# Performance work log

Measured on AMD Instinct MI355X. Metric: run time of the kernel, lower is better.

Reference implementation:

```python
import jax, jax.numpy as jnp
import numpy as np

N = 100000   # graph nodes (TSP edges)
E = 600000   # graph edges
IN_DIM = 2; HID = 128; HEADS = 16; DH = HID // HEADS
L = 4; FF = 2 * HID; OUT = 1
EPS = 1e-5; SLOPE = 0.2  # BatchNorm eps, GAT leaky_relu slope


def _mlp(x, W1, b1, W2, b2):
    return jnp.maximum(x @ W1 + b1, 0.0) @ W2 + b2


def _bn(x, g, b):
    # BatchNorm1d in training mode: batch (node-dim) statistics, biased variance
    mu = x.mean(0)
    var = x.var(0)
    return (x - mu) * jax.lax.rsqrt(var + EPS) * g + b


def _gat(h, src, dst, W, al, ar, bias):
    # DGL GATConv: per-head projection, additive attention, edge softmax over incoming edges
    z = (h @ W).reshape(N, HEADS, DH)          # [N,H,Dh]
    el = (z * al).sum(-1)                      # [N,H] source term
    er = (z * ar).sum(-1)                      # [N,H] dest term
    e = jax.nn.leaky_relu(el[src] + er[dst], SLOPE)            # [E,H]
    m = jax.ops.segment_max(e, dst, num_segments=N)            # [N,H]
    a = jnp.exp(e - m[dst])                                    # [E,H]
    denom = jax.ops.segment_sum(a, dst, num_segments=N)        # [N,H]
    msg = jax.ops.segment_sum(a[:, :, None] * z[src], dst, num_segments=N)  # [N,H,Dh]
    out = msg / jnp.where(denom > 0, denom, 1.0)[:, :, None]
    return out.reshape(N, HID) + bias


def _forward(x, src, dst,
             emb_W1, emb_b1, emb_W2, emb_b2, emb_Ws, emb_bs,
             gat_W, gat_al, gat_ar, gat_b, bn1_g, bn1_b,
             ff_W1, ff_b1, ff_W2, ff_b2, bn2_g, bn2_b,
             dec_W1, dec_b1, dec_W2, dec_b2):
    # embed MLP with skip connection
    h = _mlp(x, emb_W1, emb_b1, emb_W2, emb_b2) + (x @ emb_Ws + emb_bs)
    xs = [h]
    for l in range(L):  # fixed small layer count
        a = _gat(h, src, dst, gat_W[l], gat_al[l], gat_ar[l], gat_b[l])
        h = _bn(h + a, bn1_g[l], bn1_b[l])
        f = _mlp(h, ff_W1[l], ff_b1[l], ff_W2[l], ff_b2[l])
        h = _bn(h + f, bn2_g[l], bn2_b[l])
        xs.append(h)
    hc = jnp.concatenate(xs, axis=-1)  # JumpingKnowledge 'cat' -> [N, HID*(L+1)]
    return _mlp(hc, dec_W1, dec_b1, dec_W2, dec_b2)


def setup_inputs() -> dict:
    key = jax.random.key(0)
    ks = jax.random.split(key, 20)
    w = lambda k, shape: jax.random.normal(k, shape, jnp.float32) * 0.05
    x = jax.random.normal(ks[0], (N, IN_DIM), jnp.float32)
    src = jax.random.randint(ks[1], (E,), 0, N)
    # guarantee every node has at least one incoming edge
    dst = jnp.concatenate([jnp.arange(N), jax.random.randint(ks[2], (E - N,), 0, N)])
    return {
        'x': x, 'src': src, 'dst': dst,
        'emb_W1': w(ks[3], (IN_DIM, HID)), 'emb_b1': jnp.zeros((HID,), jnp.float32),
        'emb_W2': w(ks[4], (HID, HID)),    'emb_b2': jnp.zeros((HID,), jnp.float32),
        'emb_Ws': w(ks[5], (IN_DIM, HID)), 'emb_bs': jnp.zeros((HID,), jnp.float32),
        'gat_W': w(ks[6], (L, HID, HID)),
        'gat_al': w(ks[7], (L, HEADS, DH)), 'gat_ar': w(ks[8], (L, HEADS, DH)),
        'gat_b': jnp.zeros((L, HID), jnp.float32),
        'bn1_g': jnp.ones((L, HID), jnp.float32), 'bn1_b': jnp.zeros((L, HID), jnp.float32),
        'ff_W1': w(ks[9], (L, HID, FF)),  'ff_b1': jnp.zeros((L, FF), jnp.float32),
        'ff_W2': w(ks[10], (L, FF, HID)), 'ff_b2': jnp.zeros((L, HID), jnp.float32),
        'bn2_g': jnp.ones((L, HID), jnp.float32), 'bn2_b': jnp.zeros((L, HID), jnp.float32),
        'dec_W1': w(ks[11], (HID * (L + 1), HID)), 'dec_b1': jnp.zeros((HID,), jnp.float32),
        'dec_W2': w(ks[12], (HID, OUT)),           'dec_b2': jnp.zeros((OUT,), jnp.float32),
    }


def reference(x, src, dst,
              emb_W1, emb_b1, emb_W2, emb_b2, emb_Ws, emb_bs,
              gat_W, gat_al, gat_ar, gat_b, bn1_g, bn1_b,
              ff_W1, ff_b1, ff_W2, ff_b2, bn2_g, bn2_b,
              dec_W1, dec_b1, dec_W2, dec_b2):
    return _forward(x, src, dst,
                    emb_W1, emb_b1, emb_W2, emb_b2, emb_Ws, emb_bs,
                    gat_W, gat_al, gat_ar, gat_b, bn1_g, bn1_b,
                    ff_W1, ff_b1, ff_W2, ff_b2, bn2_g, bn2_b,
                    dec_W1, dec_b1, dec_W2, dec_b2)
```

## Files before the change

### kernel.cpp

```cpp
#include <hip/hip_runtime.h>
#include <math.h>

typedef __attribute__((ext_vector_type(8))) short bf16x8;
typedef __attribute__((ext_vector_type(4))) float f32x4;

struct BN5 {
    const float* st[5];
    const float* g[5];
    const float* b[5];
    const float* stR;
    const float* gR;
    const float* bR;
    float invN;
};

static __device__ __forceinline__ short f2bf(float f) {
    unsigned u = __float_as_uint(f);
    unsigned r = (u + 0x7fffu + ((u >> 16) & 1u)) >> 16;
    return (short)r;
}
static __device__ __forceinline__ float bf2f(short s) {
    return __uint_as_float(((unsigned)(unsigned short)s) << 16);
}
static __device__ __forceinline__ float bflo(int v) { return bf2f((short)(v & 0xffff)); }
static __device__ __forceinline__ float bfhi(int v) { return bf2f((short)(((unsigned)v) >> 16)); }
static __device__ __forceinline__ int pack2(float a, float b) {
    return (int)(((unsigned)(unsigned short)f2bf(b) << 16) | (unsigned)(unsigned short)f2bf(a));
}

__global__ void zero_i32_k(int* __restrict__ p, int n) {
    int i = blockIdx.x * 256 + threadIdx.x;
    if (i < n) p[i] = 0;
}

__global__ __launch_bounds__(256) void wconv_k(const float* __restrict__ W, short* __restrict__ Wt,
                                               int K, int Nc) {
    int slice = blockIdx.y;
    const float* src = W + (size_t)slice * K * Nc;
    short* dst = Wt + (size_t)slice * K * Nc;
    int idx = blockIdx.x * 256 + threadIdx.x;
    if (idx >= K * Nc) return;
    int k = idx / Nc, n = idx - k * Nc;
    dst[(size_t)n * K + k] = f2bf(src[idx]);
}

__global__ __launch_bounds__(256) void embed_k(
    const float* __restrict__ x, const float* __restrict__ W1, const float* __restrict__ b1,
    const float* __restrict__ Ws, const float* __restrict__ bs,
    int* __restrict__ u2, int* __restrict__ h2, int Nn)
{
    int idx = blockIdx.x * 256 + threadIdx.x;
    if (idx >= Nn * 64) return;
    int n = idx >> 6, c = (idx & 63) * 2;
    float x0 = x[2*n], x1 = x[2*n+1];
    float u0 = fmaxf(fmaf(x1, W1[128+c],   fmaf(x0, W1[c],   b1[c])),   0.f);
    float u1 = fmaxf(fmaf(x1, W1[128+c+1], fmaf(x0, W1[c+1], b1[c+1])), 0.f);
    float h0 = fmaf(x1, Ws[128+c],   fmaf(x0, Ws[c],   bs[c]));
    float h1 = fmaf(x1, Ws[128+c+1], fmaf(x0, Ws[c+1], bs[c+1]));
    u2[idx] = pack2(u0, u1);
    h2[idx] = pack2(h0, h1);
}

template<int NK, int RELU, int BETA, int ELR>
__global__ __launch_bounds__(256) void gemm2_k(
    const short* __restrict__ A0, const short* __restrict__ A1,
    const short* __restrict__ A2, const short* __restrict__ A3,
    const short* __restrict__ A4, int Astr,
    const short* __restrict__ Wt, int ldWt,
    const float* __restrict__ bias, short* __restrict__ C, const short* __restrict__ Rres,
    int Nrows, int ldC, BN5 bn,
    const float* __restrict__ al, const float* __restrict__ ar,
    float* __restrict__ elo, float* __restrict__ ero)
{
    __shared__ short Bs[128][136];
    const int row0 = blockIdx.x * 128;
    const int col0 = blockIdx.y * 128;
    const int t = threadIdx.x;
    const int w = t >> 6, lane = t & 63, q = lane >> 4, m = lane & 15;

    f32x4 acc[2][8];
    #pragma unroll
    for (int rb = 0; rb < 2; ++rb)
        #pragma unroll
        for (int cb = 0; cb < 8; ++cb)
            acc[rb][cb] = (f32x4){0.f, 0.f, 0.f, 0.f};

    const short* Asrc[5] = {A0, A1, A2, A3, A4};
    int rr0 = row0 + w*32 + m;      if (rr0 > Nrows - 1) rr0 = Nrows - 1;
    int rr1 = row0 + w*32 + 16 + m; if (rr1 > Nrows - 1) rr1 = Nrows - 1;

    #pragma unroll
    for (int kh = 0; kh < NK; ++kh) {
        if (kh) __syncthreads();
        #pragma unroll
        for (int it = 0; it < 8; ++it) {
            int ci = t + it * 256;
            int r = ci >> 4, j = (ci & 15) * 8;
            *(int4*)&Bs[r][j] = *(const int4*)(Wt + (size_t)(col0 + r) * ldWt + kh * 128 + j);
        }
        const short* pa0 = Asrc[kh] + (size_t)rr0 * Astr + q * 8;
        const short* pa1 = Asrc[kh] + (size_t)rr1 * Astr + q * 8;
        bf16x8 af0[4], af1[4];
        #pragma unroll
        for (int ks = 0; ks < 4; ++ks) {
            af0[ks] = *(const bf16x8*)(pa0 + ks * 32);
            af1[ks] = *(const bf16x8*)(pa1 + ks * 32);
        }
        if (bn.st[kh]) {
            const float* st = bn.st[kh];
            const float* gg = bn.g[kh];
            const float* bb = bn.b[kh];
            #pragma unroll
            for (int ks = 0; ks < 4; ++ks) {
                #pragma unroll
                for (int e = 0; e < 8; ++e) {
                    int c = ks * 32 + q * 8 + e;
                    float mu = st[c] * bn.invN;
                    float var = st[128 + c] * bn.invN - mu * mu;
                    float sc = rsqrtf(var + 1e-5f) * gg[c];
                    float bc = bb[c] - mu * sc;
                    af0[ks][e] = f2bf(fmaf(bf2f(af0[ks][e]), sc, bc));
                    af1[ks][e] = f2bf(fmaf(bf2f(af1[ks][e]), sc, bc));
                }
            }
        }
        __syncthreads();
        #pragma unroll
        for (int ks = 0; ks < 4; ++ks) {
            bf16x8 bfr[8];
            #pragma unroll
            for (int cb = 0; cb < 8; ++cb)
                bfr[cb] = *(const bf16x8*)&Bs[cb * 16 + m][ks * 32 + q * 8];
            #pragma unroll
            for (int cb = 0; cb < 8; ++cb) {
                acc[0][cb] = __builtin_amdgcn_mfma_f32_16x16x32_bf16(af0[ks], bfr[cb], acc[0][cb], 0, 0, 0);
                acc[1][cb] = __builtin_amdgcn_mfma_f32_16x16x32_bf16(af1[ks], bfr[cb], acc[1][cb], 0, 0, 0);
            }
        }
    }

    __syncthreads();
    short* Cs = (short*)Bs;
    #pragma unroll
    for (int rb = 0; rb < 2; ++rb) {
        #pragma unroll
        for (int r = 0; r < 4; ++r) {
            int lrow = w * 32 + rb * 16 + q * 4 + r;
            #pragma unroll
            for (int cb = 0; cb < 8; ++cb) {
                float v = acc[rb][cb][r];
                if (bias) v += bias[col0 + cb * 16 + m];
                if (RELU) v = fmaxf(v, 0.f);
                Cs[lrow * 132 + cb * 16 + m] = f2bf(v);
            }
        }
    }
    __syncthreads();
    const int chunk = t & 15, rgrp = t >> 4, cb8 = chunk * 8;
    const short* Rd = Rres ? Rres : C;
    #pragma unroll
    for (int j = 0; j < 8; ++j) {
        int r = rgrp + j * 16;
        int grow = row0 + r;
        if (grow < Nrows) {
            int2 u0 = *(const int2*)(Cs + r * 132 + cb8);
            int2 u1 = *(const int2*)(Cs + r * 132 + cb8 + 4);
            int4 cv = make_int4(u0.x, u0.y, u1.x, u1.y);
            size_t gb = (size_t)grow * ldC + col0 + cb8;
            if (BETA) {
                int4 rv = *(const int4*)(Rd + gb);
                int* cp = (int*)&cv; const int* rp = (const int*)&rv;
                #pragma unroll
                for (int e = 0; e < 4; ++e)
                    cp[e] = pack2(bflo(cp[e]) + bflo(rp[e]), bfhi(cp[e]) + bfhi(rp[e]));
            }
            *(int4*)(C + gb) = cv;
            if (ELR) {
                const int* cp = (const int*)&cv;
                float sl = 0.f, sr = 0.f;
                #pragma unroll
                for (int e = 0; e < 4; ++e) {
                    float lo = bflo(cp[e]), hi = bfhi(cp[e]);
                    sl = fmaf(lo, al[cb8 + 2*e], sl); sl = fmaf(hi, al[cb8 + 2*e + 1], sl);
                    sr = fmaf(lo, ar[cb8 + 2*e], sr); sr = fmaf(hi, ar[cb8 + 2*e + 1], sr);
                }
                elo[(size_t)grow * 16 + chunk] = sl;
                ero[(size_t)grow * 16 + chunk] = sr;
            }
        }
    }
}

__global__ __launch_bounds__(256) void ff_fused_k(
    const short* __restrict__ T1,
    const short* __restrict__ W1t,
    const short* __restrict__ W2t,
    const float* __restrict__ b1, const float* __restrict__ b2,
    const float* __restrict__ st1, const float* __restrict__ g1, const float* __restrict__ bb1,
    float invN, short* __restrict__ C, int Nrows, float* __restrict__ statsOut)
{
    __shared__ short Wbuf[128][136];
    __shared__ short Fbuf[128 * 132];
    const int row0 = blockIdx.x * 128;
    const int t = threadIdx.x;
    const int w = t >> 6, lane = t & 63, q = lane >> 4, m = lane & 15;

    f32x4 acc2[2][8];
    #pragma unroll
    for (int rb = 0; rb < 2; ++rb)
        #pragma unroll
        for (int cb = 0; cb < 8; ++cb)
            acc2[rb][cb] = (f32x4){0.f, 0.f, 0.f, 0.f};

    int rr0 = row0 + w*32 + m;      if (rr0 > Nrows - 1) rr0 = Nrows - 1;
    int rr1 = row0 + w*32 + 16 + m; if (rr1 > Nrows - 1) rr1 = Nrows - 1;

    bf16x8 af0[4], af1[4];
    {
        const short* pa0 = T1 + (size_t)rr0 * 128 + q * 8;
        const short* pa1 = T1 + (size_t)rr1 * 128 + q * 8;
        #pragma unroll
        for (int ks = 0; ks < 4; ++ks) {
            af0[ks] = *(const bf16x8*)(pa0 + ks * 32);
            af1[ks] = *(const bf16x8*)(pa1 + ks * 32);
        }
        #pragma unroll
        for (int ks = 0; ks < 4; ++ks) {
            #pragma unroll
            for (int e = 0; e < 8; ++e) {
                int c = ks * 32 + q * 8 + e;
                float mu = st1[c] * invN;
                float var = st1[128 + c] * invN - mu * mu;
                float sc = rsqrtf(var + 1e-5f) * g1[c];
                float bc = bb1[c] - mu * sc;
                af0[ks][e] = f2bf(fmaf(bf2f(af0[ks][e]), sc, bc));
                af1[ks][e] = f2bf(fmaf(bf2f(af1[ks][e]), sc, bc));
            }
        }
    }

    #pragma unroll
    for (int half = 0; half < 2; ++half) {
        if (half) __syncthreads();
        #pragma unroll
        for (int it = 0; it < 8; ++it) {
            int ci = t + it * 256;
            int r = ci >> 4, j = (ci & 15) * 8;
            *(int4*)&Wbuf[r][j] = *(const int4*)(W1t + (size_t)(half * 128 + r) * 128 + j);
        }
        __syncthreads();
        f32x4 acc1[2][8];
        #pragma unroll
        for (int rb = 0; rb < 2; ++rb)
            #pragma unroll
            for (int cb = 0; cb < 8; ++cb)
                acc1[rb][cb] = (f32x4){0.f, 0.f, 0.f, 0.f};
        #pragma unroll
        for (int ks = 0; ks < 4; ++ks) {
            bf16x8 bfr[8];
            #pragma unroll
            for (int cb = 0; cb < 8; ++cb)
                bfr[cb] = *(const bf16x8*)&Wbuf[cb * 16 + m][ks * 32 + q * 8];
            #pragma unroll
            for (int cb = 0; cb < 8; ++cb) {
                acc1[0][cb] = __builtin_amdgcn_mfma_f32_16x16x32_bf16(af0[ks], bfr[cb], acc1[0][cb], 0, 0, 0);
                acc1[1][cb] = __builtin_amdgcn_mfma_f32_16x16x32_bf16(af1[ks], bfr[cb], acc1[1][cb], 0, 0, 0);
            }
        }
        #pragma unroll
        for (int rb = 0; rb < 2; ++rb) {
            #pragma unroll
            for (int r = 0; r < 4; ++r) {
                int lrow = w * 32 + rb * 16 + q * 4 + r;
                #pragma unroll
                for (int cb = 0; cb < 8; ++cb) {
                    float v = acc1[rb][cb][r] + b1[half * 128 + cb * 16 + m];
                    Fbuf[lrow * 132 + cb * 16 + m] = f2bf(fmaxf(v, 0.f));
                }
            }
        }
        __syncthreads();
        #pragma unroll
        for (int it = 0; it < 8; ++it) {
            int ci = t + it * 256;
            int r = ci >> 4, j = (ci & 15) * 8;
            *(int4*)&Wbuf[r][j] = *(const int4*)(W2t + (size_t)r * 256 + half * 128 + j);
        }
        __syncthreads();
        const short* fa0 = Fbuf + (w * 32 + m) * 132 + q * 8;
        const short* fa1 = Fbuf + (w * 32 + 16 + m) * 132 + q * 8;
        #pragma unroll
        for (int ks = 0; ks < 4; ++ks) {
            bf16x8 ga0 = *(const bf16x8*)(fa0 + ks * 32);
            bf16x8 ga1 = *(const bf16x8*)(fa1 + ks * 32);
            bf16x8 bfr[8];
            #pragma unroll
            for (int cb = 0; cb < 8; ++cb)
                bfr[cb] = *(const bf16x8*)&Wbuf[cb * 16 + m][ks * 32 + q * 8];
            #pragma unroll
            for (int cb = 0; cb < 8; ++cb) {
                acc2[0][cb] = __builtin_amdgcn_mfma_f32_16x16x32_bf16(ga0, bfr[cb], acc2[0][cb], 0, 0, 0);
                acc2[1][cb] = __builtin_amdgcn_mfma_f32_16x16x32_bf16(ga1, bfr[cb], acc2[1][cb], 0, 0, 0);
            }
        }
    }

    __syncthreads();
    #pragma unroll
    for (int rb = 0; rb < 2; ++rb) {
        #pragma unroll
        for (int r = 0; r < 4; ++r) {
            int lrow = w * 32 + rb * 16 + q * 4 + r;
            #pragma unroll
            for (int cb = 0; cb < 8; ++cb) {
                float v = acc2[rb][cb][r] + b2[cb * 16 + m];
                Fbuf[lrow * 132 + cb * 16 + m] = f2bf(v);
            }
        }
    }
    __syncthreads();
    const int chunk = t & 15, rgrp = t >> 4, cb8 = chunk * 8;
    float scR[8], bbR[8];
    #pragma unroll
    for (int e = 0; e < 8; ++e) {
        int c = cb8 + e;
        float mu = st1[c] * invN;
        float var = st1[128 + c] * invN - mu * mu;
        float sc = rsqrtf(var + 1e-5f) * g1[c];
        scR[e] = sc; bbR[e] = bb1[c] - mu * sc;
    }
    float sS[8], sQ[8];
    #pragma unroll
    for (int e = 0; e < 8; ++e) { sS[e] = 0.f; sQ[e] = 0.f; }
    #pragma unroll
    for (int j = 0; j < 8; ++j) {
        int r = rgrp + j * 16;
        int grow = row0 + r;
        if (grow < Nrows) {
            int2 u0 = *(const int2*)(Fbuf + r * 132 + cb8);
            int2 u1 = *(const int2*)(Fbuf + r * 132 + cb8 + 4);
            int4 cv = make_int4(u0.x, u0.y, u1.x, u1.y);
            size_t gb = (size_t)grow * 128 + cb8;
            int4 rv = *(const int4*)(T1 + gb);
            int* cp = (int*)&cv; const int* rp = (const int*)&rv;
            #pragma unroll
            for (int e = 0; e < 4; ++e) {
                float rlo = fmaf(bflo(rp[e]), scR[2*e],   bbR[2*e]);
                float rhi = fmaf(bfhi(rp[e]), scR[2*e+1], bbR[2*e+1]);
                float lo = bflo(cp[e]) + rlo;
                float hi = bfhi(cp[e]) + rhi;
                cp[e] = pack2(lo, hi);
                lo = bflo(cp[e]); hi = bfhi(cp[e]);
                sS[2*e]   += lo; sQ[2*e]   += lo * lo;
                sS[2*e+1] += hi; sQ[2*e+1] += hi * hi;
            }
            *(int4*)(C + gb) = cv;
        }
    }
    __syncthreads();
    float* fs = (float*)Wbuf;
    #pragma unroll
    for (int e = 0; e < 8; ++e) {
        fs[rgrp * 128 + cb8 + e]        = sS[e];
        fs[2048 + rgrp * 128 + cb8 + e] = sQ[e];
    }
    __syncthreads();
    if (t < 128) {
        float a = 0.f;
        #pragma unroll
        for (int g = 0; g < 16; ++g) a += fs[g * 128 + t];
        atomicAdd(&statsOut[t], a);
    } else {
        int c = t - 128;
        float a = 0.f;
        #pragma unroll
        for (int g = 0; g < 16; ++g) a += fs[2048 + g * 128 + c];
        atomicAdd(&statsOut[128 + c], a);
    }
}

__global__ void count_k(const int* __restrict__ dst, int* __restrict__ cnt, int E) {
    int e = blockIdx.x * 256 + threadIdx.x;
    if (e < E) atomicAdd(&cnt[dst[e]], 1);
}

__global__ __launch_bounds__(256) void scan_part_k(const int* __restrict__ cnt,
                                                   int* __restrict__ bsum, int Nn) {
    __shared__ int red[256];
    int base = blockIdx.x * 1024;
    int s = 0;
    for (int i = threadIdx.x; i < 1024; i += 256) {
        int g = base + i;
        if (g < Nn) s += cnt[g];
    }
    red[threadIdx.x] = s; __syncthreads();
    for (int off = 128; off; off >>= 1) {
        if ((int)threadIdx.x < off) red[threadIdx.x] += red[threadIdx.x + off];
        __syncthreads();
    }
    if (threadIdx.x == 0) bsum[blockIdx.x] = red[0];
}

__global__ __launch_bounds__(256) void scan_top_k(int* __restrict__ bsum, int nb) {
    __shared__ int buf[256];
    int v = ((int)threadIdx.x < nb) ? bsum[threadIdx.x] : 0;
    buf[threadIdx.x] = v; __syncthreads();
    for (int off = 1; off < 256; off <<= 1) {
        int tv = ((int)threadIdx.x >= off) ? buf[threadIdx.x - off] : 0;
        __syncthreads();
        buf[threadIdx.x] += tv;
        __syncthreads();
    }
    if ((int)threadIdx.x < nb) bsum[threadIdx.x] = buf[threadIdx.x] - v;
}

__global__ __launch_bounds__(256) void scan_fin_k(const int* __restrict__ cnt,
    const int* __restrict__ bsum, int* __restrict__ rowptr, int* __restrict__ wpos, int Nn)
{
    __shared__ int tsum[256];
    int base = blockIdx.x * 1024;
    int g0 = base + (int)threadIdx.x * 4;
    int v[4]; int s = 0;
    #pragma unroll
    for (int j = 0; j < 4; ++j) {
        int g = g0 + j;
        v[j] = (g < Nn) ? cnt[g] : 0;
        s += v[j];
    }
    tsum[threadIdx.x] = s; __syncthreads();
    for (int off = 1; off < 256; off <<= 1) {
        int tv = ((int)threadIdx.x >= off) ? tsum[threadIdx.x - off] : 0;
        __syncthreads();
        tsum[threadIdx.x] += tv;
        __syncthreads();
    }
    int run = bsum[blockIdx.x] + tsum[threadIdx.x] - s;
    #pragma unroll
    for (int j = 0; j < 4; ++j) {
        int g = g0 + j;
        if (g < Nn) { wpos[g] = run; rowptr[g + 1] = run + v[j]; }
        run += v[j];
    }
    if (blockIdx.x == 0 && threadIdx.x == 0) rowptr[0] = 0;
}

__global__ void scatter_k(const int* __restrict__ src, const int* __restrict__ dst,
                          int* __restrict__ wpos, int* __restrict__ esrc, int E) {
    int e = blockIdx.x * 256 + threadIdx.x;
    if (e < E) {
        int p = atomicAdd(&wpos[dst[e]], 1);
        esrc[p] = src[e];
    }
}

__global__ __launch_bounds__(256) void gat_k(
    const short* __restrict__ h, const short* __restrict__ z,
    const float* __restrict__ el, const float* __restrict__ er,
    const int* __restrict__ rowptr, const int* __restrict__ esrc,
    const float* __restrict__ gbias, short* __restrict__ t1, int Nn,
    const float* __restrict__ hstats, const float* __restrict__ hg,
    const float* __restrict__ hb, float invN)
{
    int gw = (blockIdx.x * 256 + threadIdx.x) >> 6;
    if (gw >= Nn) return;
    int lane = threadIdx.x & 63;
    int c = lane * 2;
    int head = lane >> 2;
    float ern = er[gw*16 + head];
    int beg = rowptr[gw], end = rowptr[gw+1];
    float m = -3.0e38f, den = 0.f, a0 = 0.f, a1 = 0.f;
    int i = beg;
    for (; i + 3 < end; i += 4) {
        int s0 = esrc[i], s1 = esrc[i+1], s2 = esrc[i+2], s3 = esrc[i+3];
        float e0 = el[s0*16 + head] + ern;
        float e1 = el[s1*16 + head] + ern;
        float e2 = el[s2*16 + head] + ern;
        float e3 = el[s3*16 + head] + ern;
        int zz0 = *(const int*)(z + (size_t)s0*128 + c);
        int zz1 = *(const int*)(z + (size_t)s1*128 + c);
        int zz2 = *(const int*)(z + (size_t)s2*128 + c);
        int zz3 = *(const int*)(z + (size_t)s3*128 + c);
        e0 = (e0 > 0.f) ? e0 : 0.2f * e0;
        e1 = (e1 > 0.f) ? e1 : 0.2f * e1;
        e2 = (e2 > 0.f) ? e2 : 0.2f * e2;
        e3 = (e3 > 0.f) ? e3 : 0.2f * e3;
        float nm = fmaxf(fmaxf(fmaxf(e0, e1), fmaxf(e2, e3)), m);
        float sc = __expf(m - nm);
        float w0 = __expf(e0 - nm), w1 = __expf(e1 - nm);
        float w2 = __expf(e2 - nm), w3 = __expf(e3 - nm);
        den = fmaf(den, sc, (w0 + w1) + (w2 + w3));
        a0 = fmaf(a0, sc, fmaf(w0, bflo(zz0), fmaf(w1, bflo(zz1), fmaf(w2, bflo(zz2), w3 * bflo(zz3)))));
        a1 = fmaf(a1, sc, fmaf(w0, bfhi(zz0), fmaf(w1, bfhi(zz1), fmaf(w2, bfhi(zz2), w3 * bfhi(zz3)))));
        m = nm;
    }
    for (; i + 1 < end; i += 2) {
        int s0 = esrc[i], s1 = esrc[i+1];
        float e0 = el[s0*16 + head] + ern;
        float e1 = el[s1*16 + head] + ern;
        int zz0 = *(const int*)(z + (size_t)s0*128 + c);
        int zz1 = *(const int*)(z + (size_t)s1*128 + c);
        e0 = (e0 > 0.f) ? e0 : 0.2f * e0;
        e1 = (e1 > 0.f) ? e1 : 0.2f * e1;
        float nm = fmaxf(m, fmaxf(e0, e1));
        float sc = __expf(m - nm);
        float w0 = __expf(e0 - nm);
        float w1 = __expf(e1 - nm);
        den = fmaf(den, sc, w0 + w1);
        a0  = fmaf(a0, sc, fmaf(w0, bflo(zz0), w1 * bflo(zz1)));
        a1  = fmaf(a1, sc, fmaf(w0, bfhi(zz0), w1 * bfhi(zz1)));
        m = nm;
    }
    if (i < end) {
        int s0 = esrc[i];
        float e0 = el[s0*16 + head] + ern;
        int zz0 = *(const int*)(z + (size_t)s0*128 + c);
        e0 = (e0 > 0.f) ? e0 : 0.2f * e0;
        float nm = fmaxf(m, e0);
        float sc = __expf(m - nm);
        float w0 = __expf(e0 - nm);
        den = fmaf(den, sc, w0);
        a0  = fmaf(a0, sc, w0 * bflo(zz0));
        a1  = fmaf(a1, sc, w0 * bfhi(zz0));
    }
    float inv = 1.f / den;
    size_t o = (size_t)gw*64 + lane;
    int hv = ((const int*)h)[o];
    float h0 = bflo(hv), h1 = bfhi(hv);
    if (hstats) {
        float mu0 = hstats[c] * invN;
        float v0  = hstats[128+c] * invN - mu0*mu0;
        float s0  = rsqrtf(v0 + 1e-5f) * hg[c];
        h0 = fmaf(h0 - mu0, s0, hb[c]);
        float mu1 = hstats[c+1] * invN;
        float v1  = hstats[128+c+1] * invN - mu1*mu1;
        float s1  = rsqrtf(v1 + 1e-5f) * hg[c+1];
        h1 = fmaf(h1 - mu1, s1, hb[c+1]);
    }
    float r0 = h0 + a0*inv + gbias[c];
    float r1 = h1 + a1*inv + gbias[c+1];
    ((int*)t1)[o] = pack2(r0, r1);
}

__global__ __launch_bounds__(256) void bn_stats_k(const short* __restrict__ xin,
    float* __restrict__ stats, int Nn)
{
    __shared__ float s0s[256], s1s[256], q0s[256], q1s[256];
    int pair = threadIdx.x & 63;
    int slot = threadIdx.x >> 6;
    float s0 = 0.f, s1 = 0.f, q0 = 0.f, q1 = 0.f;
    for (int r = blockIdx.x*4 + slot; r < Nn; r += gridDim.x*4) {
        int v = *(const int*)(xin + (size_t)r*128 + pair*2);
        float a = bflo(v), b = bfhi(v);
        s0 += a; s1 += b;
        q0 = fmaf(a, a, q0); q1 = fmaf(b, b, q1);
    }
    s0s[threadIdx.x] = s0; s1s[threadIdx.x] = s1;
    q0s[threadIdx.x] = q0; q1s[threadIdx.x] = q1;
    __syncthreads();
    if (slot == 0) {
        #pragma unroll
        for (int j = 1; j < 4; ++j) {
            s0 += s0s[pair + j*64]; s1 += s1s[pair + j*64];
            q0 += q0s[pair + j*64]; q1 += q1s[pair + j*64];
        }
        atomicAdd(&stats[pair*2],       s0);
        atomicAdd(&stats[pair*2+1],     s1);
        atomicAdd(&stats[128+pair*2],   q0);
        atomicAdd(&stats[128+pair*2+1], q1);
    }
}

__global__ __launch_bounds__(256) void dec_out_k(const short* __restrict__ udec,
    const float* __restrict__ W2, const float* __restrict__ b2,
    float* __restrict__ out, int Nn)
{
    int gw = (blockIdx.x * 256 + threadIdx.x) >> 6;
    if (gw >= Nn) return;
    int lane = threadIdx.x & 63;
    int v = ((const int*)(udec + (size_t)gw * 128))[lane];
    float p = bflo(v) * W2[lane*2] + bfhi(v) * W2[lane*2 + 1];
    #pragma unroll
    for (int off = 32; off > 0; off >>= 1) p += __shfl_down(p, off);
    if (lane == 0) out[gw] = p + b2[0];
}

extern "C" void kernel_launch(void* const* d_in, const int* in_sizes, int n_in,
                              void* d_out, int out_size, void* d_ws, size_t ws_size,
                              hipStream_t stream)
{
    const float* x      = (const float*)d_in[0];
    const int*   src    = (const int*)  d_in[1];
    const int*   dst    = (const int*)  d_in[2];
    const float* emb_W1 = (const float*)d_in[3];
    const float* emb_b1 = (const float*)d_in[4];
    const float* emb_W2 = (const float*)d_in[5];
    const float* emb_b2 = (const float*)d_in[6];
    const float* emb_Ws = (const float*)d_in[7];
    const float* emb_bs = (const float*)d_in[8];
    const float* gat_W  = (const float*)d_in[9];
    const float* gat_al = (const float*)d_in[10];
    const float* gat_ar = (const float*)d_in[11];
    const float* gat_b  = (const float*)d_in[12];
    const float* bn1_g  = (const float*)d_in[13];
    const float* bn1_b  = (const float*)d_in[14];
    const float* ff_W1  = (const float*)d_in[15];
    const float* ff_b1  = (const float*)d_in[16];
    const float* ff_W2  = (const float*)d_in[17];
    const float* ff_b2  = (const float*)d_in[18];
    const float* bn2_g  = (const float*)d_in[19];
    const float* bn2_b  = (const float*)d_in[20];
    const float* dec_W1 = (const float*)d_in[21];
    const float* dec_b1 = (const float*)d_in[22];
    const float* dec_W2 = (const float*)d_in[23];
    const float* dec_b2 = (const float*)d_in[24];
    float* out = (float*)d_out;
    (void)n_in; (void)out_size;

    const int N = in_sizes[0] / 2;
    const int E = in_sizes[1];
    const float invN = 1.f / (float)N;

    char* p = (char*)d_ws;
    size_t used = 0;
    auto carve = [&](size_t bytes) {
        char* r = p; size_t a = (bytes + 255) & ~(size_t)255;
        p += a; used += a; return r;
    };
    const size_t nbH = (size_t)N * 128 * 2;
    short* xs[5];
    for (int i = 0; i < 5; ++i) xs[i] = (short*)carve(nbH);
    short* t1   = (short*)carve(nbH);
    char*  big  = (char*)carve(2 * nbH);
    int*   cnt    = (int*)carve((size_t)N * 4);
    float* stats8 = (float*)carve(8 * 256 * 4);
    int*   rowptr = (int*)carve((size_t)(N + 1) * 4);
    int*   wpos   = (int*)carve((size_t)N * 4);
    int*   esrc   = (int*)carve((size_t)E * 4);
    int*   bsum   = (int*)carve(256 * 4);
    short* emb_W2t = (short*)carve((size_t)128 * 128 * 2);
    short* gat_Wt  = (short*)carve((size_t)4 * 128 * 128 * 2);
    short* ff_W1t  = (short*)carve((size_t)4 * 128 * 256 * 2);
    short* ff_W2t  = (short*)carve((size_t)4 * 256 * 128 * 2);
    short* dec_W1t = (short*)carve((size_t)640 * 128 * 2);
    if (used > ws_size) return;

    short* u    = (short*)big;
    short* z    = (short*)big;
    float* el   = (float*)(big + nbH);
    float* er   = el + (size_t)N * 16;
    short* udec = (short*)big;

    dim3 b256(256);
    int ecb  = (E + 255) / 256;
    int nel2 = (N * 64 + 255) / 256;
    int gx   = (N + 127) / 128;
    int nwv  = (N + 3) / 4;
    int nb   = (N + 1023) / 1024;

    BN5 bn0;
    for (int i = 0; i < 5; ++i) { bn0.st[i] = nullptr; bn0.g[i] = nullptr; bn0.b[i] = nullptr; }
    bn0.stR = nullptr; bn0.gR = nullptr; bn0.bR = nullptr; bn0.invN = invN;

    wconv_k<<<dim3(64, 1), b256, 0, stream>>>(emb_W2, emb_W2t, 128, 128);
    wconv_k<<<dim3(64, 4), b256, 0, stream>>>(gat_W,  gat_Wt,  128, 128);
    wconv_k<<<dim3(128, 4), b256, 0, stream>>>(ff_W1, ff_W1t,  128, 256);
    wconv_k<<<dim3(128, 4), b256, 0, stream>>>(ff_W2, ff_W2t,  256, 128);
    wconv_k<<<dim3(320, 1), b256, 0, stream>>>(dec_W1, dec_W1t, 640, 128);

    {
        int ztot = (int)(((char*)(stats8 + 8*256) - (char*)cnt) / 4);
        zero_i32_k<<<(ztot + 255) / 256, b256, 0, stream>>>(cnt, ztot);
    }

    count_k<<<ecb, b256, 0, stream>>>(dst, cnt, E);
    scan_part_k<<<nb, b256, 0, stream>>>(cnt, bsum, N);
    scan_top_k<<<1, b256, 0, stream>>>(bsum, nb);
    scan_fin_k<<<nb, b256, 0, stream>>>(cnt, bsum, rowptr, wpos, N);
    scatter_k<<<ecb, b256, 0, stream>>>(src, dst, wpos, esrc, E);

    embed_k<<<nel2, b256, 0, stream>>>(x, emb_W1, emb_b1, emb_Ws, emb_bs, (int*)u, (int*)xs[0], N);
    gemm2_k<1,0,1,0><<<dim3(gx,1), b256, 0, stream>>>(u,u,u,u,u, 128, emb_W2t, 128,
        emb_b2, xs[0], nullptr, N, 128, bn0, nullptr, nullptr, nullptr, nullptr);

    for (int l = 0; l < 4; ++l) {
        float* st1 = stats8 + (size_t)(l*2)   * 256;
        float* st2 = stats8 + (size_t)(l*2+1) * 256;
        short* hl = xs[l];
        const float* hst = (l == 0) ? nullptr : stats8 + (size_t)((l-1)*2+1) * 256;
        const float* hgp = (l == 0) ? nullptr : bn2_g + (l-1)*128;
        const float* hbp = (l == 0) ? nullptr : bn2_b + (l-1)*128;

        BN5 bz = bn0; bz.st[0] = hst; bz.g[0] = hgp; bz.b[0] = hbp;
        gemm2_k<1,0,0,1><<<dim3(gx,1), b256, 0, stream>>>(hl,hl,hl,hl,hl, 128,
            gat_Wt + (size_t)l*128*128, 128, nullptr, z, nullptr, N, 128, bz,
            gat_al + l*128, gat_ar + l*128, el, er);
        gat_k<<<nwv, b256, 0, stream>>>(hl, z, el, er, rowptr, esrc, gat_b + l*128, t1, N,
                                        hst, hgp, hbp, invN);
        bn_stats_k<<<400, b256, 0, stream>>>(t1, st1, N);
        ff_fused_k<<<gx, b256, 0, stream>>>(t1,
            ff_W1t + (size_t)l*128*256, ff_W2t + (size_t)l*256*128,
            ff_b1 + l*256, ff_b2 + l*128,
            st1, bn1_g + l*128, bn1_b + l*128, invN,
            xs[l+1], N, st2);
    }

    BN5 bd = bn0;
    for (int k = 1; k < 5; ++k) {
        bd.st[k] = stats8 + (size_t)((k-1)*2+1) * 256;
        bd.g[k]  = bn2_g + (k-1)*128;
        bd.b[k]  = bn2_b + (k-1)*128;
    }
    gemm2_k<5,1,0,0><<<dim3(gx,1), b256, 0, stream>>>(xs[0], xs[1], xs[2], xs[3], xs[4], 128,
        dec_W1t, 640, dec_b1, udec, nullptr, N, 128, bd,
        nullptr, nullptr, nullptr, nullptr);
    dec_out_k<<<nwv, b256, 0, stream>>>(udec, dec_W2, dec_b2, out, N);
}
```

Before: 1.062 ms.

## Fuse decoder output projection into decoder GEMM and shrink FF kernel LDS

The decoder's final 128->1 projection now runs in the epilogue of the decoder GEMM as a per-row dot product with a shared-memory reduction. This removes the write and re-read of the intermediate decoder activations and one kernel launch. The fused FF kernel now processes its hidden dimension in four 64-wide quarters instead of two 128-wide halves, which reduces its shared memory and register footprint. It also declares launch bounds of three blocks per CU to raise occupancy, at the cost of more barriers and W-tile reloads.

```diff
diff --git a/kernel.cpp b/kernel.cpp
--- a/kernel.cpp
+++ b/kernel.cpp
@@ -8,9 +8,6 @@
     const float* st[5];
     const float* g[5];
     const float* b[5];
-    const float* stR;
-    const float* gR;
-    const float* bR;
     float invN;
 };
 
@@ -61,7 +58,7 @@
     h2[idx] = pack2(h0, h1);
 }
 
-template<int NK, int RELU, int BETA, int ELR>
+template<int NK, int RELU, int BETA, int ELR, int DEC>
 __global__ __launch_bounds__(256) void gemm2_k(
     const short* __restrict__ A0, const short* __restrict__ A1,
     const short* __restrict__ A2, const short* __restrict__ A3,
@@ -70,7 +67,8 @@
     const float* __restrict__ bias, short* __restrict__ C, const short* __restrict__ Rres,
     int Nrows, int ldC, BN5 bn,
     const float* __restrict__ al, const float* __restrict__ ar,
-    float* __restrict__ elo, float* __restrict__ ero)
+    float* __restrict__ elo, float* __restrict__ ero,
+    const float* __restrict__ dW2, const float* __restrict__ db2, float* __restrict__ dout)
 {
     __shared__ short Bs[128][136];
     const int row0 = blockIdx.x * 128;
@@ -158,6 +156,11 @@
     __syncthreads();
     const int chunk = t & 15, rgrp = t >> 4, cb8 = chunk * 8;
     const short* Rd = Rres ? Rres : C;
+    float dp[8];
+    if (DEC) {
+        #pragma unroll
+        for (int j = 0; j < 8; ++j) dp[j] = 0.f;
+    }
     #pragma unroll
     for (int j = 0; j < 8; ++j) {
         int r = rgrp + j * 16;
@@ -174,7 +177,7 @@
                 for (int e = 0; e < 4; ++e)
                     cp[e] = pack2(bflo(cp[e]) + bflo(rp[e]), bfhi(cp[e]) + bfhi(rp[e]));
             }
-            *(int4*)(C + gb) = cv;
+            if (!DEC) *(int4*)(C + gb) = cv;
             if (ELR) {
                 const int* cp = (const int*)&cv;
                 float sl = 0.f, sr = 0.f;
@@ -187,11 +190,38 @@
                 elo[(size_t)grow * 16 + chunk] = sl;
                 ero[(size_t)grow * 16 + chunk] = sr;
             }
-        }
-    }
-}
-
-__global__ __launch_bounds__(256) void ff_fused_k(
+            if (DEC) {
+                const int* cp = (const int*)&cv;
+                float s = 0.f;
+                #pragma unroll
+                for (int e = 0; e < 4; ++e) {
+                    s = fmaf(bflo(cp[e]), dW2[cb8 + 2*e],     s);
+                    s = fmaf(bfhi(cp[e]), dW2[cb8 + 2*e + 1], s);
+                }
+                dp[j] = s;
+            }
+        }
+    }
+    if (DEC) {
+        __syncthreads();
+        float* red = (float*)Bs;
+        #pragma unroll
+        for (int j = 0; j < 8; ++j)
+            red[(rgrp + j * 16) * 16 + chunk] = dp[j];
+        __syncthreads();
+        if (t < 128) {
+            int grow = row0 + t;
+            if (grow < Nrows) {
+                float s = 0.f;
+                #pragma unroll
+                for (int g = 0; g < 16; ++g) s += red[t * 16 + g];
+                dout[grow] = s + db2[0];
+            }
+        }
+    }
+}
+
+__global__ __launch_bounds__(256, 3) void ff_fused_k(
     const short* __restrict__ T1,
     const short* __restrict__ W1t,
     const short* __restrict__ W2t,
@@ -199,8 +229,9 @@
     const float* __restrict__ st1, const float* __restrict__ g1, const float* __restrict__ bb1,
     float invN, short* __restrict__ C, int Nrows, float* __restrict__ statsOut)
 {
-    __shared__ short Wbuf[128][136];
-    __shared__ short Fbuf[128 * 132];
+    __shared__ short smem[17920];
+    short* Wb = smem;
+    short* Fb = smem + 9216;
     const int row0 = blockIdx.x * 128;
     const int t = threadIdx.x;
     const int w = t >> 6, lane = t & 63, q = lane >> 4, m = lane & 15;
@@ -239,30 +270,29 @@
         }
     }
 
-    #pragma unroll
-    for (int half = 0; half < 2; ++half) {
-        if (half) __syncthreads();
-        #pragma unroll
-        for (int it = 0; it < 8; ++it) {
+    for (int qt = 0; qt < 4; ++qt) {
+        if (qt) __syncthreads();
+        #pragma unroll
+        for (int it = 0; it < 4; ++it) {
             int ci = t + it * 256;
             int r = ci >> 4, j = (ci & 15) * 8;
-            *(int4*)&Wbuf[r][j] = *(const int4*)(W1t + (size_t)(half * 128 + r) * 128 + j);
-        }
-        __syncthreads();
-        f32x4 acc1[2][8];
+            *(int4*)&Wb[r * 136 + j] = *(const int4*)(W1t + (size_t)(qt * 64 + r) * 128 + j);
+        }
+        __syncthreads();
+        f32x4 acc1[2][4];
         #pragma unroll
         for (int rb = 0; rb < 2; ++rb)
             #pragma unroll
-            for (int cb = 0; cb < 8; ++cb)
+            for (int cb = 0; cb < 4; ++cb)
                 acc1[rb][cb] = (f32x4){0.f, 0.f, 0.f, 0.f};
         #pragma unroll
         for (int ks = 0; ks < 4; ++ks) {
-            bf16x8 bfr[8];
-            #pragma unroll
-            for (int cb = 0; cb < 8; ++cb)
-                bfr[cb] = *(const bf16x8*)&Wbuf[cb * 16 + m][ks * 32 + q * 8];
-            #pragma unroll
-            for (int cb = 0; cb < 8; ++cb) {
+            bf16x8 bfr[4];
+            #pragma unroll
+            for (int cb = 0; cb < 4; ++cb)
+                bfr[cb] = *(const bf16x8*)&Wb[(cb * 16 + m) * 136 + ks * 32 + q * 8];
+            #pragma unroll
+            for (int cb = 0; cb < 4; ++cb) {
                 acc1[0][cb] = __builtin_amdgcn_mfma_f32_16x16x32_bf16(af0[ks], bfr[cb], acc1[0][cb], 0, 0, 0);
                 acc1[1][cb] = __builtin_amdgcn_mfma_f32_16x16x32_bf16(af1[ks], bfr[cb], acc1[1][cb], 0, 0, 0);
             }
@@ -273,30 +303,30 @@
             for (int r = 0; r < 4; ++r) {
                 int lrow = w * 32 + rb * 16 + q * 4 + r;
                 #pragma unroll
-                for (int cb = 0; cb < 8; ++cb) {
-                    float v = acc1[rb][cb][r] + b1[half * 128 + cb * 16 + m];
-                    Fbuf[lrow * 132 + cb * 16 + m] = f2bf(fmaxf(v, 0.f));
+                for (int cb = 0; cb < 4; ++cb) {
+                    float v = acc1[rb][cb][r] + b1[qt * 64 + cb * 16 + m];
+                    Fb[lrow * 68 + cb * 16 + m] = f2bf(fmaxf(v, 0.f));
                 }
             }
         }
         __syncthreads();
         #pragma unroll
-        for (int it = 0; it < 8; ++it) {
+        for (int it = 0; it < 4; ++it) {
             int ci = t + it * 256;
-            int r = ci >> 4, j = (ci & 15) * 8;
-            *(int4*)&Wbuf[r][j] = *(const int4*)(W2t + (size_t)r * 256 + half * 128 + j);
-        }
-        __syncthreads();
-        const short* fa0 = Fbuf + (w * 32 + m) * 132 + q * 8;
-        const short* fa1 = Fbuf + (w * 32 + 16 + m) * 132 + q * 8;
-        #pragma unroll
-        for (int ks = 0; ks < 4; ++ks) {
+            int r = ci >> 3, j = (ci & 7) * 8;
+            *(int4*)&Wb[r * 72 + j] = *(const int4*)(W2t + (size_t)r * 256 + qt * 64 + j);
+        }
+        __syncthreads();
+        const short* fa0 = Fb + (w * 32 + m) * 68 + q * 8;
+        const short* fa1 = Fb + (w * 32 + 16 + m) * 68 + q * 8;
+        #pragma unroll
+        for (int ks = 0; ks < 2; ++ks) {
             bf16x8 ga0 = *(const bf16x8*)(fa0 + ks * 32);
             bf16x8 ga1 = *(const bf16x8*)(fa1 + ks * 32);
             bf16x8 bfr[8];
             #pragma unroll
             for (int cb = 0; cb < 8; ++cb)
-                bfr[cb] = *(const bf16x8*)&Wbuf[cb * 16 + m][ks * 32 + q * 8];
+                bfr[cb] = *(const bf16x8*)&Wb[(cb * 16 + m) * 72 + ks * 32 + q * 8];
             #pragma unroll
             for (int cb = 0; cb < 8; ++cb) {
                 acc2[0][cb] = __builtin_amdgcn_mfma_f32_16x16x32_bf16(ga0, bfr[cb], acc2[0][cb], 0, 0, 0);
@@ -314,7 +344,7 @@
             #pragma unroll
             for (int cb = 0; cb < 8; ++cb) {
                 float v = acc2[rb][cb][r] + b2[cb * 16 + m];
-                Fbuf[lrow * 132 + cb * 16 + m] = f2bf(v);
+                smem[lrow * 132 + cb * 16 + m] = f2bf(v);
             }
         }
     }
@@ -337,8 +367,8 @@
         int r = rgrp + j * 16;
         int grow = row0 + r;
         if (grow < Nrows) {
-            int2 u0 = *(const int2*)(Fbuf + r * 132 + cb8);
-            int2 u1 = *(const int2*)(Fbuf + r * 132 + cb8 + 4);
+            int2 u0 = *(const int2*)(smem + r * 132 + cb8);
+            int2 u1 = *(const int2*)(smem + r * 132 + cb8 + 4);
             int4 cv = make_int4(u0.x, u0.y, u1.x, u1.y);
             size_t gb = (size_t)grow * 128 + cb8;
             int4 rv = *(const int4*)(T1 + gb);
@@ -358,7 +388,7 @@
         }
     }
     __syncthreads();
-    float* fs = (float*)Wbuf;
+    float* fs = (float*)smem;
     #pragma unroll
     for (int e = 0; e < 8; ++e) {
         fs[rgrp * 128 + cb8 + e]        = sS[e];
@@ -570,20 +600,6 @@
     }
 }
 
-__global__ __launch_bounds__(256) void dec_out_k(const short* __restrict__ udec,
-    const float* __restrict__ W2, const float* __restrict__ b2,
-    float* __restrict__ out, int Nn)
-{
-    int gw = (blockIdx.x * 256 + threadIdx.x) >> 6;
-    if (gw >= Nn) return;
-    int lane = threadIdx.x & 63;
-    int v = ((const int*)(udec + (size_t)gw * 128))[lane];
-    float p = bflo(v) * W2[lane*2] + bfhi(v) * W2[lane*2 + 1];
-    #pragma unroll
-    for (int off = 32; off > 0; off >>= 1) p += __shfl_down(p, off);
-    if (lane == 0) out[gw] = p + b2[0];
-}
-
 extern "C" void kernel_launch(void* const* d_in, const int* in_sizes, int n_in,
                               void* d_out, int out_size, void* d_ws, size_t ws_size,
                               hipStream_t stream)
@@ -648,7 +664,6 @@
     short* z    = (short*)big;
     float* el   = (float*)(big + nbH);
     float* er   = el + (size_t)N * 16;
-    short* udec = (short*)big;
 
     dim3 b256(256);
     int ecb  = (E + 255) / 256;
@@ -659,7 +674,7 @@
 
     BN5 bn0;
     for (int i = 0; i < 5; ++i) { bn0.st[i] = nullptr; bn0.g[i] = nullptr; bn0.b[i] = nullptr; }
-    bn0.stR = nullptr; bn0.gR = nullptr; bn0.bR = nullptr; bn0.invN = invN;
+    bn0.invN = invN;
 
     wconv_k<<<dim3(64, 1), b256, 0, stream>>>(emb_W2, emb_W2t, 128, 128);
     wconv_k<<<dim3(64, 4), b256, 0, stream>>>(gat_W,  gat_Wt,  128, 128);
@@ -679,8 +694,9 @@
     scatter_k<<<ecb, b256, 0, stream>>>(src, dst, wpos, esrc, E);
 
     embed_k<<<nel2, b256, 0, stream>>>(x, emb_W1, emb_b1, emb_Ws, emb_bs, (int*)u, (int*)xs[0], N);
-    gemm2_k<1,0,1,0><<<dim3(gx,1), b256, 0, stream>>>(u,u,u,u,u, 128, emb_W2t, 128,
-        emb_b2, xs[0], nullptr, N, 128, bn0, nullptr, nullptr, nullptr, nullptr);
+    gemm2_k<1,0,1,0,0><<<dim3(gx,1), b256, 0, stream>>>(u,u,u,u,u, 128, emb_W2t, 128,
+        emb_b2, xs[0], nullptr, N, 128, bn0, nullptr, nullptr, nullptr, nullptr,
+        nullptr, nullptr, nullptr);
 
     for (int l = 0; l < 4; ++l) {
         float* st1 = stats8 + (size_t)(l*2)   * 256;
@@ -691,9 +707,9 @@
         const float* hbp = (l == 0) ? nullptr : bn2_b + (l-1)*128;
 
         BN5 bz = bn0; bz.st[0] = hst; bz.g[0] = hgp; bz.b[0] = hbp;
-        gemm2_k<1,0,0,1><<<dim3(gx,1), b256, 0, stream>>>(hl,hl,hl,hl,hl, 128,
+        gemm2_k<1,0,0,1,0><<<dim3(gx,1), b256, 0, stream>>>(hl,hl,hl,hl,hl, 128,
             gat_Wt + (size_t)l*128*128, 128, nullptr, z, nullptr, N, 128, bz,
-            gat_al + l*128, gat_ar + l*128, el, er);
+            gat_al + l*128, gat_ar + l*128, el, er, nullptr, nullptr, nullptr);
         gat_k<<<nwv, b256, 0, stream>>>(hl, z, el, er, rowptr, esrc, gat_b + l*128, t1, N,
                                         hst, hgp, hbp, invN);
         bn_stats_k<<<400, b256, 0, stream>>>(t1, st1, N);
@@ -710,8 +726,7 @@
         bd.g[k]  = bn2_g + (k-1)*128;
         bd.b[k]  = bn2_b + (k-1)*128;
     }
-    gemm2_k<5,1,0,0><<<dim3(gx,1), b256, 0, stream>>>(xs[0], xs[1], xs[2], xs[3], xs[4], 128,
-        dec_W1t, 640, dec_b1, udec, nullptr, N, 128, bd,
-        nullptr, nullptr, nullptr, nullptr);
-    dec_out_k<<<nwv, b256, 0, stream>>>(udec, dec_W2, dec_b2, out, N);
-}
+    gemm2_k<5,1,0,0,1><<<dim3(gx,1), b256, 0, stream>>>(xs[0], xs[1], xs[2], xs[3], xs[4], 128,
+        dec_W1t, 640, dec_b1, xs[0], nullptr, N, 128, bd,
+        nullptr, nullptr, nullptr, nullptr, dec_W2, dec_b2, out);
+}
```

Measured after the change: 1.095 ms. 3.1% more time.

## Fuse BN statistics into GAT aggregation kernel and merge weight conversions

Applied to the files above, without the earlier changes.

The GAT aggregation kernel now gives each 256-thread block 64 destination nodes, processed four at a time (one per wavefront). It accumulates per-channel sum and sum-of-squares of its bf16-rounded outputs, reduces them in shared memory and adds them to the stats buffer with atomics. This removes the separate bn_stats_k pass that re-read t1 once per layer. The five weight-transpose launches are merged into one kernel, and the input-BN scale and shift are precomputed once per thread. In exchange there are 16x fewer blocks for the irregular gather work, so wavefronts in a block can wait on each other at the barrier, and there are more atomics (about 1563 blocks instead of 400).

```diff
diff --git a/kernel.cpp b/kernel.cpp
--- a/kernel.cpp
+++ b/kernel.cpp
@@ -8,9 +8,6 @@
     const float* st[5];
     const float* g[5];
     const float* b[5];
-    const float* stR;
-    const float* gR;
-    const float* bR;
     float invN;
 };
 
@@ -33,15 +30,37 @@
     if (i < n) p[i] = 0;
 }
 
-__global__ __launch_bounds__(256) void wconv_k(const float* __restrict__ W, short* __restrict__ Wt,
-                                               int K, int Nc) {
-    int slice = blockIdx.y;
-    const float* src = W + (size_t)slice * K * Nc;
-    short* dst = Wt + (size_t)slice * K * Nc;
-    int idx = blockIdx.x * 256 + threadIdx.x;
-    if (idx >= K * Nc) return;
-    int k = idx / Nc, n = idx - k * Nc;
-    dst[(size_t)n * K + k] = f2bf(src[idx]);
+__global__ __launch_bounds__(256) void wconv_all_k(
+    const float* __restrict__ emb, const float* __restrict__ gat,
+    const float* __restrict__ ff1, const float* __restrict__ ff2,
+    const float* __restrict__ dec,
+    short* __restrict__ embT, short* __restrict__ gatT,
+    short* __restrict__ ff1T, short* __restrict__ ff2T, short* __restrict__ decT)
+{
+    int gid = blockIdx.x * 256 + threadIdx.x;
+    if (gid < 16384) {
+        int k = gid >> 7, n = gid & 127;
+        embT[n * 128 + k] = f2bf(emb[gid]);
+    } else if (gid < 81920) {
+        int local = gid - 16384;
+        int sl = local >> 14, rem = local & 16383;
+        int k = rem >> 7, n = rem & 127;
+        gatT[sl * 16384 + n * 128 + k] = f2bf(gat[local]);
+    } else if (gid < 212992) {
+        int local = gid - 81920;
+        int sl = local >> 15, rem = local & 32767;
+        int k = rem >> 8, n = rem & 255;
+        ff1T[sl * 32768 + n * 128 + k] = f2bf(ff1[local]);
+    } else if (gid < 344064) {
+        int local = gid - 212992;
+        int sl = local >> 15, rem = local & 32767;
+        int k = rem >> 7, n = rem & 127;
+        ff2T[sl * 32768 + n * 256 + k] = f2bf(ff2[local]);
+    } else if (gid < 425984) {
+        int local = gid - 344064;
+        int k = local >> 7, n = local & 127;
+        decT[n * 640 + k] = f2bf(dec[local]);
+    }
 }
 
 __global__ __launch_bounds__(256) void embed_k(
@@ -459,114 +478,109 @@
     const int* __restrict__ rowptr, const int* __restrict__ esrc,
     const float* __restrict__ gbias, short* __restrict__ t1, int Nn,
     const float* __restrict__ hstats, const float* __restrict__ hg,
-    const float* __restrict__ hb, float invN)
+    const float* __restrict__ hb, float invN, float* __restrict__ statsOut)
 {
-    int gw = (blockIdx.x * 256 + threadIdx.x) >> 6;
-    if (gw >= Nn) return;
-    int lane = threadIdx.x & 63;
-    int c = lane * 2;
-    int head = lane >> 2;
-    float ern = er[gw*16 + head];
-    int beg = rowptr[gw], end = rowptr[gw+1];
-    float m = -3.0e38f, den = 0.f, a0 = 0.f, a1 = 0.f;
-    int i = beg;
-    for (; i + 3 < end; i += 4) {
-        int s0 = esrc[i], s1 = esrc[i+1], s2 = esrc[i+2], s3 = esrc[i+3];
-        float e0 = el[s0*16 + head] + ern;
-        float e1 = el[s1*16 + head] + ern;
-        float e2 = el[s2*16 + head] + ern;
-        float e3 = el[s3*16 + head] + ern;
-        int zz0 = *(const int*)(z + (size_t)s0*128 + c);
-        int zz1 = *(const int*)(z + (size_t)s1*128 + c);
-        int zz2 = *(const int*)(z + (size_t)s2*128 + c);
-        int zz3 = *(const int*)(z + (size_t)s3*128 + c);
-        e0 = (e0 > 0.f) ? e0 : 0.2f * e0;
-        e1 = (e1 > 0.f) ? e1 : 0.2f * e1;
-        e2 = (e2 > 0.f) ? e2 : 0.2f * e2;
-        e3 = (e3 > 0.f) ? e3 : 0.2f * e3;
-        float nm = fmaxf(fmaxf(fmaxf(e0, e1), fmaxf(e2, e3)), m);
-        float sc = __expf(m - nm);
-        float w0 = __expf(e0 - nm), w1 = __expf(e1 - nm);
-        float w2 = __expf(e2 - nm), w3 = __expf(e3 - nm);
-        den = fmaf(den, sc, (w0 + w1) + (w2 + w3));
-        a0 = fmaf(a0, sc, fmaf(w0, bflo(zz0), fmaf(w1, bflo(zz1), fmaf(w2, bflo(zz2), w3 * bflo(zz3)))));
-        a1 = fmaf(a1, sc, fmaf(w0, bfhi(zz0), fmaf(w1, bfhi(zz1), fmaf(w2, bfhi(zz2), w3 * bfhi(zz3)))));
-        m = nm;
-    }
-    for (; i + 1 < end; i += 2) {
-        int s0 = esrc[i], s1 = esrc[i+1];
-        float e0 = el[s0*16 + head] + ern;
-        float e1 = el[s1*16 + head] + ern;
-        int zz0 = *(const int*)(z + (size_t)s0*128 + c);
-        int zz1 = *(const int*)(z + (size_t)s1*128 + c);
-        e0 = (e0 > 0.f) ? e0 : 0.2f * e0;
-        e1 = (e1 > 0.f) ? e1 : 0.2f * e1;
-        float nm = fmaxf(m, fmaxf(e0, e1));
-        float sc = __expf(m - nm);
-        float w0 = __expf(e0 - nm);
-        float w1 = __expf(e1 - nm);
-        den = fmaf(den, sc, w0 + w1);
-        a0  = fmaf(a0, sc, fmaf(w0, bflo(zz0), w1 * bflo(zz1)));
-        a1  = fmaf(a1, sc, fmaf(w0, bfhi(zz0), w1 * bfhi(zz1)));
-        m = nm;
-    }
-    if (i < end) {
-        int s0 = esrc[i];
-        float e0 = el[s0*16 + head] + ern;
-        int zz0 = *(const int*)(z + (size_t)s0*128 + c);
-        e0 = (e0 > 0.f) ? e0 : 0.2f * e0;
-        float nm = fmaxf(m, e0);
-        float sc = __expf(m - nm);
-        float w0 = __expf(e0 - nm);
-        den = fmaf(den, sc, w0);
-        a0  = fmaf(a0, sc, w0 * bflo(zz0));
-        a1  = fmaf(a1, sc, w0 * bfhi(zz0));
-    }
-    float inv = 1.f / den;
-    size_t o = (size_t)gw*64 + lane;
-    int hv = ((const int*)h)[o];
-    float h0 = bflo(hv), h1 = bfhi(hv);
+    __shared__ float red[2][4][128];
+    const int t = threadIdx.x;
+    const int w = t >> 6, lane = t & 63;
+    const int c = lane * 2;
+    const int head = lane >> 2;
+
+    float gb0 = gbias[c], gb1 = gbias[c+1];
+    float hs0 = 1.f, hB0 = 0.f, hs1 = 1.f, hB1 = 0.f;
     if (hstats) {
         float mu0 = hstats[c] * invN;
         float v0  = hstats[128+c] * invN - mu0*mu0;
-        float s0  = rsqrtf(v0 + 1e-5f) * hg[c];
-        h0 = fmaf(h0 - mu0, s0, hb[c]);
+        hs0 = rsqrtf(v0 + 1e-5f) * hg[c];
+        hB0 = hb[c] - mu0 * hs0;
         float mu1 = hstats[c+1] * invN;
         float v1  = hstats[128+c+1] * invN - mu1*mu1;
-        float s1  = rsqrtf(v1 + 1e-5f) * hg[c+1];
-        h1 = fmaf(h1 - mu1, s1, hb[c+1]);
-    }
-    float r0 = h0 + a0*inv + gbias[c];
-    float r1 = h1 + a1*inv + gbias[c+1];
-    ((int*)t1)[o] = pack2(r0, r1);
-}
-
-__global__ __launch_bounds__(256) void bn_stats_k(const short* __restrict__ xin,
-    float* __restrict__ stats, int Nn)
-{
-    __shared__ float s0s[256], s1s[256], q0s[256], q1s[256];
-    int pair = threadIdx.x & 63;
-    int slot = threadIdx.x >> 6;
-    float s0 = 0.f, s1 = 0.f, q0 = 0.f, q1 = 0.f;
-    for (int r = blockIdx.x*4 + slot; r < Nn; r += gridDim.x*4) {
-        int v = *(const int*)(xin + (size_t)r*128 + pair*2);
-        float a = bflo(v), b = bfhi(v);
-        s0 += a; s1 += b;
-        q0 = fmaf(a, a, q0); q1 = fmaf(b, b, q1);
-    }
-    s0s[threadIdx.x] = s0; s1s[threadIdx.x] = s1;
-    q0s[threadIdx.x] = q0; q1s[threadIdx.x] = q1;
+        hs1 = rsqrtf(v1 + 1e-5f) * hg[c+1];
+        hB1 = hb[c+1] - mu1 * hs1;
+    }
+
+    float sS0 = 0.f, sS1 = 0.f, sQ0 = 0.f, sQ1 = 0.f;
+    int base = blockIdx.x * 64;
+    for (int it = 0; it < 16; ++it) {
+        int n = base + it * 4 + w;
+        if (n >= Nn) break;
+        float ern = er[n*16 + head];
+        int beg = rowptr[n], end = rowptr[n+1];
+        float m = -3.0e38f, den = 0.f, a0 = 0.f, a1 = 0.f;
+        int i = beg;
+        for (; i + 3 < end; i += 4) {
+            int s0 = esrc[i], s1 = esrc[i+1], s2 = esrc[i+2], s3 = esrc[i+3];
+            float e0 = el[s0*16 + head] + ern;
+            float e1 = el[s1*16 + head] + ern;
+            float e2 = el[s2*16 + head] + ern;
+            float e3 = el[s3*16 + head] + ern;
+            int zz0 = *(const int*)(z + (size_t)s0*128 + c);
+            int zz1 = *(const int*)(z + (size_t)s1*128 + c);
+            int zz2 = *(const int*)(z + (size_t)s2*128 + c);
+            int zz3 = *(const int*)(z + (size_t)s3*128 + c);
+            e0 = (e0 > 0.f) ? e0 : 0.2f * e0;
+            e1 = (e1 > 0.f) ? e1 : 0.2f * e1;
+            e2 = (e2 > 0.f) ? e2 : 0.2f * e2;
+            e3 = (e3 > 0.f) ? e3 : 0.2f * e3;
+            float nm = fmaxf(fmaxf(fmaxf(e0, e1), fmaxf(e2, e3)), m);
+            float sc = __expf(m - nm);
+            float w0 = __expf(e0 - nm), w1 = __expf(e1 - nm);
+            float w2 = __expf(e2 - nm), w3 = __expf(e3 - nm);
+            den = fmaf(den, sc, (w0 + w1) + (w2 + w3));
+            a0 = fmaf(a0, sc, fmaf(w0, bflo(zz0), fmaf(w1, bflo(zz1), fmaf(w2, bflo(zz2), w3 * bflo(zz3)))));
+            a1 = fmaf(a1, sc, fmaf(w0, bfhi(zz0), fmaf(w1, bfhi(zz1), fmaf(w2, bfhi(zz2), w3 * bfhi(zz3)))));
+            m = nm;
+        }
+        for (; i + 1 < end; i += 2) {
+            int s0 = esrc[i], s1 = esrc[i+1];
+            float e0 = el[s0*16 + head] + ern;
+            float e1 = el[s1*16 + head] + ern;
+            int zz0 = *(const int*)(z + (size_t)s0*128 + c);
+            int zz1 = *(const int*)(z + (size_t)s1*128 + c);
+            e0 = (e0 > 0.f) ? e0 : 0.2f * e0;
+            e1 = (e1 > 0.f) ? e1 : 0.2f * e1;
+            float nm = fmaxf(m, fmaxf(e0, e1));
+            float sc = __expf(m - nm);
+            float w0 = __expf(e0 - nm);
+            float w1 = __expf(e1 - nm);
+            den = fmaf(den, sc, w0 + w1);
+            a0  = fmaf(a0, sc, fmaf(w0, bflo(zz0), w1 * bflo(zz1)));
+            a1  = fmaf(a1, sc, fmaf(w0, bfhi(zz0), w1 * bfhi(zz1)));
+            m = nm;
+        }
+        if (i < end) {
+            int s0 = esrc[i];
+            float e0 = el[s0*16 + head] + ern;
+            int zz0 = *(const int*)(z + (size_t)s0*128 + c);
+            e0 = (e0 > 0.f) ? e0 : 0.2f * e0;
+            float nm = fmaxf(m, e0);
+            float sc = __expf(m - nm);
+            float w0 = __expf(e0 - nm);
+            den = fmaf(den, sc, w0);
+            a0  = fmaf(a0, sc, w0 * bflo(zz0));
+            a1  = fmaf(a1, sc, w0 * bfhi(zz0));
+        }
+        float inv = 1.f / den;
+        size_t o = (size_t)n*64 + lane;
+        int hv = ((const int*)h)[o];
+        float r0 = fmaf(bflo(hv), hs0, hB0) + a0*inv + gb0;
+        float r1 = fmaf(bfhi(hv), hs1, hB1) + a1*inv + gb1;
+        int pk = pack2(r0, r1);
+        ((int*)t1)[o] = pk;
+        float v0 = bflo(pk), v1 = bfhi(pk);
+        sS0 += v0; sQ0 = fmaf(v0, v0, sQ0);
+        sS1 += v1; sQ1 = fmaf(v1, v1, sQ1);
+    }
+    red[0][w][c] = sS0; red[0][w][c+1] = sS1;
+    red[1][w][c] = sQ0; red[1][w][c+1] = sQ1;
     __syncthreads();
-    if (slot == 0) {
-        #pragma unroll
-        for (int j = 1; j < 4; ++j) {
-            s0 += s0s[pair + j*64]; s1 += s1s[pair + j*64];
-            q0 += q0s[pair + j*64]; q1 += q1s[pair + j*64];
-        }
-        atomicAdd(&stats[pair*2],       s0);
-        atomicAdd(&stats[pair*2+1],     s1);
-        atomicAdd(&stats[128+pair*2],   q0);
-        atomicAdd(&stats[128+pair*2+1], q1);
+    if (t < 128) {
+        float a = red[0][0][t] + red[0][1][t] + red[0][2][t] + red[0][3][t];
+        atomicAdd(&statsOut[t], a);
+    } else {
+        int cc = t - 128;
+        float a = red[1][0][cc] + red[1][1][cc] + red[1][2][cc] + red[1][3][cc];
+        atomicAdd(&statsOut[128 + cc], a);
     }
 }
 
@@ -655,17 +669,16 @@
     int nel2 = (N * 64 + 255) / 256;
     int gx   = (N + 127) / 128;
     int nwv  = (N + 3) / 4;
+    int gblk = (N + 63) / 64;
     int nb   = (N + 1023) / 1024;
 
     BN5 bn0;
     for (int i = 0; i < 5; ++i) { bn0.st[i] = nullptr; bn0.g[i] = nullptr; bn0.b[i] = nullptr; }
-    bn0.stR = nullptr; bn0.gR = nullptr; bn0.bR = nullptr; bn0.invN = invN;
-
-    wconv_k<<<dim3(64, 1), b256, 0, stream>>>(emb_W2, emb_W2t, 128, 128);
-    wconv_k<<<dim3(64, 4), b256, 0, stream>>>(gat_W,  gat_Wt,  128, 128);
-    wconv_k<<<dim3(128, 4), b256, 0, stream>>>(ff_W1, ff_W1t,  128, 256);
-    wconv_k<<<dim3(128, 4), b256, 0, stream>>>(ff_W2, ff_W2t,  256, 128);
-    wconv_k<<<dim3(320, 1), b256, 0, stream>>>(dec_W1, dec_W1t, 640, 128);
+    bn0.invN = invN;
+
+    wconv_all_k<<<(425984 + 255) / 256, b256, 0, stream>>>(
+        emb_W2, gat_W, ff_W1, ff_W2, dec_W1,
+        emb_W2t, gat_Wt, ff_W1t, ff_W2t, dec_W1t);
 
     {
         int ztot = (int)(((char*)(stats8 + 8*256) - (char*)cnt) / 4);
@@ -694,9 +707,8 @@
         gemm2_k<1,0,0,1><<<dim3(gx,1), b256, 0, stream>>>(hl,hl,hl,hl,hl, 128,
             gat_Wt + (size_t)l*128*128, 128, nullptr, z, nullptr, N, 128, bz,
             gat_al + l*128, gat_ar + l*128, el, er);
-        gat_k<<<nwv, b256, 0, stream>>>(hl, z, el, er, rowptr, esrc, gat_b + l*128, t1, N,
-                                        hst, hgp, hbp, invN);
-        bn_stats_k<<<400, b256, 0, stream>>>(t1, st1, N);
+        gat_k<<<gblk, b256, 0, stream>>>(hl, z, el, er, rowptr, esrc, gat_b + l*128, t1, N,
+                                         hst, hgp, hbp, invN, st1);
         ff_fused_k<<<gx, b256, 0, stream>>>(t1,
             ff_W1t + (size_t)l*128*256, ff_W2t + (size_t)l*256*128,
             ff_b1 + l*256, ff_b2 + l*128,
```

Result: faster. 1.012 ms (-4.7%).
